# Kernel tuning notes

Hardware: AMD Instinct MI355X
Metric: run time of the kernel (lower is better)

## Reference

```python
import jax, jax.numpy as jnp
import numpy as np

EMB = 1024
HEADS = 16
HEAD_DIM = EMB // HEADS
MASK_VAL = -10000.0


def setup_inputs() -> dict:
    key = jax.random.key(0)
    ks = jax.random.split(key, 5)
    B, S = 4, 2048
    x = jax.random.normal(ks[0], (B, S, EMB), dtype=jnp.float32)
    scale = 1.0 / np.sqrt(EMB)
    w_qkv = jax.random.normal(ks[1], (EMB, 3 * EMB), dtype=jnp.float32) * scale
    b_qkv = jnp.zeros((3 * EMB,), dtype=jnp.float32)
    w_fc = jax.random.normal(ks[2], (EMB, EMB), dtype=jnp.float32) * scale
    b_fc = jnp.zeros((EMB,), dtype=jnp.float32)
    return {"x": x, "w_qkv": w_qkv, "b_qkv": b_qkv, "w_fc": w_fc, "b_fc": b_fc}


def reference(x, w_qkv, b_qkv, w_fc, b_fc):
    B, S, _ = x.shape
    qkv = x @ w_qkv + b_qkv                      # (B, S, 3*EMB)
    q, k, v = jnp.split(qkv, 3, axis=-1)
    # split heads: (B, S, EMB) -> (B, H, S, Dh)
    def sh(t):
        return t.reshape(B, S, HEADS, HEAD_DIM).transpose(0, 2, 1, 3)
    q, k, v = sh(q), sh(k), sh(v)
    scores = jnp.einsum('bhqd,bhkd->bhqk', q, k) / np.sqrt(HEAD_DIM)
    causal = jnp.tril(jnp.ones((S, S), dtype=bool))[None, None]
    scores = jnp.where(causal, scores, jnp.float32(MASK_VAL))
    probs = jax.nn.softmax(scores, axis=-1)
    out = jnp.einsum('bhqk,bhkd->bhqd', probs, v)
    out = out.transpose(0, 2, 1, 3).reshape(B, S, EMB)  # merge heads
    return out @ w_fc + b_fc
```

## Files before the change

kernel.cpp:

```cpp
#include <hip/hip_runtime.h>
#include <hip/hip_bf16.h>
#include <cstdint>

#define BF16 __hip_bfloat16

typedef __attribute__((ext_vector_type(8))) short bhalf8;
typedef __attribute__((ext_vector_type(4))) float floatx4;

#define MFMA16(a, b, c) __builtin_amdgcn_mfma_f32_16x16x32_bf16((a), (b), (c), 0, 0, 0)

#define MASKV (-30000.0f)
#define QSCALE 0.18033688011112042f

__device__ __forceinline__ bhalf8 cvt8(const float* p) {
  const float4 f0 = *(const float4*)p;
  const float4 f1 = *(const float4*)(p + 4);
  union { bhalf8 v; ushort u[8]; } r;
  const float t[8] = {f0.x, f0.y, f0.z, f0.w, f1.x, f1.y, f1.z, f1.w};
#pragma unroll
  for (int i = 0; i < 8; ++i) {
    BF16 h = __float2bfloat16(t[i]);
    r.u[i] = *(const ushort*)&h;
  }
  return r.v;
}

__global__ void cvt_f32_bf16(const float* __restrict__ in, BF16* __restrict__ out) {
  const size_t i = ((size_t)blockIdx.x * 256 + threadIdx.x) * 8;
  *(bhalf8*)(out + i) = cvt8(in + i);
}

__global__ void transpose_cvt(const float* __restrict__ in, ushort* __restrict__ out,
                              int R, int C) {
  __shared__ ushort t[32][33];
  const int c0 = blockIdx.x * 32, r0 = blockIdx.y * 32;
  const int tx = threadIdx.x, ty = threadIdx.y;
#pragma unroll
  for (int j = 0; j < 32; j += 8) {
    BF16 h = __float2bfloat16(in[(size_t)(r0 + ty + j) * C + c0 + tx]);
    t[ty + j][tx] = *(const ushort*)&h;
  }
  __syncthreads();
#pragma unroll
  for (int j = 0; j < 32; j += 8)
    out[(size_t)(c0 + ty + j) * R + r0 + tx] = t[tx][ty + j];
}

template <int MODE>
__global__ __launch_bounds__(256, 2) void gemm_bt(
    const BF16* __restrict__ A, const BF16* __restrict__ Bt, const float* __restrict__ bias,
    void* __restrict__ C0v, BF16* __restrict__ C1, BF16* __restrict__ C2,
    int Md, int Nd, int Kd) {
  __shared__ __align__(16) BF16 As[128 * 64];
  __shared__ __align__(16) BF16 Bs[128 * 64];

  const int tid = threadIdx.x;
  const int w = tid >> 6, lane = tid & 63;
  const int lm = lane & 15, quad = lane >> 4;
  const int wm = (w >> 1) * 64, wn = (w & 1) * 64;
  const int tile_m = blockIdx.y * 128, tile_n = blockIdx.x * 128;

  floatx4 acc[4][4];
#pragma unroll
  for (int i = 0; i < 4; ++i)
#pragma unroll
    for (int j = 0; j < 4; ++j) acc[i][j] = (floatx4){0.f, 0.f, 0.f, 0.f};

  int srow[4], sgs[4], sslot[4];
#pragma unroll
  for (int j = 0; j < 4; ++j) {
    const int slot = (j * 4 + w) * 64 + lane;
    sslot[j] = slot;
    srow[j] = slot >> 3;
    sgs[j] = ((slot & 7) - (slot >> 3)) & 7;
  }

  bhalf8 va[4], vb[4], nva[4], nvb[4];
#pragma unroll
  for (int j = 0; j < 4; ++j) {
    va[j] = *(const bhalf8*)(A + (size_t)(tile_m + srow[j]) * Kd + sgs[j] * 8);
    vb[j] = *(const bhalf8*)(Bt + (size_t)(tile_n + srow[j]) * Kd + sgs[j] * 8);
  }

  for (int k0 = 0; k0 < Kd; k0 += 64) {
    __syncthreads();
#pragma unroll
    for (int j = 0; j < 4; ++j) {
      *(bhalf8*)(As + sslot[j] * 8) = va[j];
      *(bhalf8*)(Bs + sslot[j] * 8) = vb[j];
    }
    __syncthreads();

    if (k0 + 64 < Kd) {
      const int k1 = k0 + 64;
#pragma unroll
      for (int j = 0; j < 4; ++j) {
        nva[j] = *(const bhalf8*)(A + (size_t)(tile_m + srow[j]) * Kd + k1 + sgs[j] * 8);
        nvb[j] = *(const bhalf8*)(Bt + (size_t)(tile_n + srow[j]) * Kd + k1 + sgs[j] * 8);
      }
    }

#pragma unroll
    for (int s = 0; s < 2; ++s) {
      bhalf8 af[4], bfr[4];
#pragma unroll
      for (int mt = 0; mt < 4; ++mt) {
        const int r = wm + mt * 16 + lm;
        const int g = ((s * 4 + quad) + r) & 7;
        af[mt] = *(const bhalf8*)(As + r * 64 + g * 8);
      }
#pragma unroll
      for (int nt = 0; nt < 4; ++nt) {
        const int r = wn + nt * 16 + lm;
        const int g = ((s * 4 + quad) + r) & 7;
        bfr[nt] = *(const bhalf8*)(Bs + r * 64 + g * 8);
      }
#pragma unroll
      for (int mt = 0; mt < 4; ++mt)
#pragma unroll
        for (int nt = 0; nt < 4; ++nt)
          acc[mt][nt] = MFMA16(af[mt], bfr[nt], acc[mt][nt]);
    }
#pragma unroll
    for (int j = 0; j < 4; ++j) { va[j] = nva[j]; vb[j] = nvb[j]; }
  }

#pragma unroll
  for (int nt = 0; nt < 4; ++nt) {
    const int n = tile_n + wn + nt * 16 + lm;
    const float bv = bias[n];
#pragma unroll
    for (int mt = 0; mt < 4; ++mt) {
      const int m0 = tile_m + wm + mt * 16 + quad * 4;
      floatx4 v = acc[mt][nt];
      if (MODE == 0) {
        float* C0f = (float*)C0v;
#pragma unroll
        for (int r = 0; r < 4; ++r)
          C0f[(size_t)(m0 + r) * Nd + n] = v[r] + bv;
      } else {
        const int which = n >> 10;
        const int h = (n >> 6) & 15;
        const int d = n & 63;
        if (which == 2) {
          const int b = m0 >> 11, s0 = m0 & 2047;
          union { ushort4 u4; ushort u[4]; } pk;
#pragma unroll
          for (int r = 0; r < 4; ++r) {
            BF16 hv = __float2bfloat16(v[r] + bv);
            pk.u[r] = *(const ushort*)&hv;
          }
          *(ushort4*)(C2 + ((size_t)((b * 16 + h) * 64 + d)) * 2048 + s0) = pk.u4;
        } else {
          BF16* dst = (which == 0) ? (BF16*)C0v : C1;
          const float sc = (which == 0) ? QSCALE : 1.0f;
#pragma unroll
          for (int r = 0; r < 4; ++r) {
            const int m = m0 + r, b = m >> 11, si = m & 2047;
            dst[((size_t)(b * 16 + h) * 2048 + si) * 64 + d] =
                __float2bfloat16((v[r] + bv) * sc);
          }
        }
      }
    }
  }
}

__global__ __launch_bounds__(256, 2) void flash_attn(
    const BF16* __restrict__ Q, const BF16* __restrict__ Kmat,
    const BF16* __restrict__ VT, BF16* __restrict__ O) {
  __shared__ __align__(16) BF16 Ks[64 * 64];
  __shared__ __align__(16) BF16 Vs[64 * 64];
  __shared__ __align__(16) BF16 Ps[4 * 16 * 64];

  const int bh = blockIdx.y;
  const int qt = (int)gridDim.x - 1 - (int)blockIdx.x;
  const int tid = threadIdx.x;
  const int w = tid >> 6, lane = tid & 63;
  const int lm = lane & 15, quad = lane >> 4;
  const size_t bh_off = (size_t)bh * (2048 * 64);

  const int qrow = qt * 64 + w * 16 + lm;
  const bhalf8 aq0 = *(const bhalf8*)(Q + bh_off + (size_t)qrow * 64 + quad * 8);
  const bhalf8 aq1 = *(const bhalf8*)(Q + bh_off + (size_t)qrow * 64 + 32 + quad * 8);

  floatx4 oacc[4];
#pragma unroll
  for (int i = 0; i < 4; ++i) oacc[i] = (floatx4){0.f, 0.f, 0.f, 0.f};
  float m_i = MASKV, l_i = 0.f;

  int srow[2], sgs[2], sslot[2];
#pragma unroll
  for (int j = 0; j < 2; ++j) {
    const int slot = (w * 2 + j) * 64 + lane;
    sslot[j] = slot;
    srow[j] = slot >> 3;
    sgs[j] = ((slot & 7) - (slot >> 3)) & 7;
  }
  BF16* pw = Ps + w * (16 * 64);

  bhalf8 kv[2], vv[2], nkv[2], nvv[2];
  {
    const BF16* Kg = Kmat + bh_off;
    const BF16* Vg = VT + bh_off;
#pragma unroll
    for (int j = 0; j < 2; ++j) {
      kv[j] = *(const bhalf8*)(Kg + srow[j] * 64 + sgs[j] * 8);
      vv[j] = *(const bhalf8*)(Vg + (size_t)srow[j] * 2048 + sgs[j] * 8);
    }
  }

  for (int kt = 0; kt <= qt; ++kt) {
    __syncthreads();
#pragma unroll
    for (int j = 0; j < 2; ++j) {
      *(bhalf8*)(Ks + sslot[j] * 8) = kv[j];
      *(bhalf8*)(Vs + sslot[j] * 8) = vv[j];
    }
    __syncthreads();

    if (kt < qt) {
      const BF16* Kg = Kmat + bh_off + (size_t)((kt + 1) * 64) * 64;
      const BF16* Vg = VT + bh_off + (kt + 1) * 64;
#pragma unroll
      for (int j = 0; j < 2; ++j) {
        nkv[j] = *(const bhalf8*)(Kg + srow[j] * 64 + sgs[j] * 8);
        nvv[j] = *(const bhalf8*)(Vg + (size_t)srow[j] * 2048 + sgs[j] * 8);
      }
    }

    floatx4 st[4];
#pragma unroll
    for (int nt = 0; nt < 4; ++nt) {
      const int rr = nt * 16 + lm;
      const bhalf8 ak0 = *(const bhalf8*)(Ks + rr * 64 + ((quad + rr) & 7) * 8);
      const bhalf8 ak1 = *(const bhalf8*)(Ks + rr * 64 + ((4 + quad + rr) & 7) * 8);
      floatx4 z = (floatx4){0.f, 0.f, 0.f, 0.f};
      z = MFMA16(ak0, aq0, z);
      z = MFMA16(ak1, aq1, z);
      st[nt] = z;
    }

    if (kt == qt) {
#pragma unroll
      for (int nt = 0; nt < 4; ++nt)
#pragma unroll
        for (int r = 0; r < 4; ++r)
          if ((nt * 16 + quad * 4 + r) > (w * 16 + lm)) st[nt][r] = MASKV;
    }

    float mx = MASKV;
#pragma unroll
    for (int nt = 0; nt < 4; ++nt)
#pragma unroll
      for (int r = 0; r < 4; ++r) mx = fmaxf(mx, st[nt][r]);
    mx = fmaxf(mx, __shfl_xor(mx, 16, 64));
    mx = fmaxf(mx, __shfl_xor(mx, 32, 64));
    const float mnew = fmaxf(m_i, mx);
    const float alpha = __builtin_amdgcn_exp2f(m_i - mnew);
    m_i = mnew;

    float rs = 0.f;
#pragma unroll
    for (int nt = 0; nt < 4; ++nt)
#pragma unroll
      for (int r = 0; r < 4; ++r) {
        const float p = __builtin_amdgcn_exp2f(st[nt][r] - mnew);
        st[nt][r] = p;
        rs += p;
      }
    rs += __shfl_xor(rs, 16, 64);
    rs += __shfl_xor(rs, 32, 64);
    l_i = l_i * alpha + rs;
#pragma unroll
    for (int dn = 0; dn < 4; ++dn) oacc[dn] *= alpha;

#pragma unroll
    for (int nt = 0; nt < 4; ++nt) {
      union { ushort4 u4; ushort u[4]; } pk;
#pragma unroll
      for (int r = 0; r < 4; ++r) {
        BF16 h = __float2bfloat16(st[nt][r]);
        pk.u[r] = *(const ushort*)&h;
      }
      const int g = ((nt * 2 + (quad >> 1)) + lm) & 7;
      *(ushort4*)(pw + lm * 64 + g * 8 + (quad & 1) * 4) = pk.u4;
    }

    const bhalf8 ap0 = *(const bhalf8*)(pw + lm * 64 + ((quad + lm) & 7) * 8);
    const bhalf8 ap1 = *(const bhalf8*)(pw + lm * 64 + ((4 + quad + lm) & 7) * 8);
#pragma unroll
    for (int dn = 0; dn < 4; ++dn) {
      const int rr = dn * 16 + lm;
      const bhalf8 av0 = *(const bhalf8*)(Vs + rr * 64 + ((quad + rr) & 7) * 8);
      const bhalf8 av1 = *(const bhalf8*)(Vs + rr * 64 + ((4 + quad + rr) & 7) * 8);
      oacc[dn] = MFMA16(av0, ap0, oacc[dn]);
      oacc[dn] = MFMA16(av1, ap1, oacc[dn]);
    }

#pragma unroll
    for (int j = 0; j < 2; ++j) { kv[j] = nkv[j]; vv[j] = nvv[j]; }
  }

  const int b = bh >> 4, h = bh & 15;
  const float inv_l = 1.0f / l_i;
#pragma unroll
  for (int dn = 0; dn < 4; ++dn) {
    union { ushort4 u4; ushort u[4]; } pk;
#pragma unroll
    for (int r = 0; r < 4; ++r) {
      BF16 h2 = __float2bfloat16(oacc[dn][r] * inv_l);
      pk.u[r] = *(const ushort*)&h2;
    }
    *(ushort4*)(O + ((size_t)(b * 2048 + qt * 64 + w * 16 + lm)) * 1024 +
                h * 64 + dn * 16 + quad * 4) = pk.u4;
  }
}

extern "C" void kernel_launch(void* const* d_in, const int* in_sizes, int n_in,
                              void* d_out, int out_size, void* d_ws, size_t ws_size,
                              hipStream_t stream) {
  const float* x = (const float*)d_in[0];
  const float* w_qkv = (const float*)d_in[1];
  const float* b_qkv = (const float*)d_in[2];
  const float* w_fc = (const float*)d_in[3];
  const float* b_fc = (const float*)d_in[4];
  float* out = (float*)d_out;

  BF16* ws = (BF16*)d_ws;
  BF16* wTqkv = ws;
  BF16* wTfc = wTqkv + 3072 * 1024;
  BF16* xb = wTfc + 1024 * 1024;
  BF16* Qb = xb + 8388608;
  BF16* Kb = Qb + 8388608;
  BF16* VTb = Kb + 8388608;
  BF16* Ob = VTb + 8388608;

  cvt_f32_bf16<<<4096, 256, 0, stream>>>(x, xb);
  transpose_cvt<<<dim3(96, 32), dim3(32, 8), 0, stream>>>(w_qkv, (ushort*)wTqkv, 1024, 3072);
  transpose_cvt<<<dim3(32, 32), dim3(32, 8), 0, stream>>>(w_fc, (ushort*)wTfc, 1024, 1024);

  gemm_bt<1><<<dim3(24, 64), 256, 0, stream>>>(
      xb, wTqkv, b_qkv, (void*)Qb, Kb, VTb, 8192, 3072, 1024);
  flash_attn<<<dim3(32, 64), 256, 0, stream>>>(Qb, Kb, VTb, Ob);
  gemm_bt<0><<<dim3(8, 64), 256, 0, stream>>>(
      Ob, wTfc, b_fc, (void*)out, nullptr, nullptr, 8192, 1024, 1024);
}
```

Before: 294.0 us.

## Use async global-to-LDS loads in GEMM and 128-row query tiles in attention

The GEMM now loads its A and B tiles straight into LDS with global_load_lds. This replaces the register-staged path that prefetched the next K-slice while the current one was computing. The flash-attention kernel now gives each block 128 query rows and each wave 32 rows in two 16-row sub-tiles. That halves K/V tile loads per query row and doubles MFMA work per LDS tile, at the cost of more registers, a larger P buffer, and coarser causal load balance. The GEMM loses its explicit prefetch overlap and depends on the barrier waiting for the async LDS writes.

New measurement: 309.3 us. 5.2% more time.

```diff
diff --git a/kernel.cpp b/kernel.cpp
--- a/kernel.cpp
+++ b/kernel.cpp
@@ -11,6 +11,12 @@
 
 #define MASKV (-30000.0f)
 #define QSCALE 0.18033688011112042f
+
+__device__ __forceinline__ void async_cp16(const void* gsrc, void* ldst) {
+  __builtin_amdgcn_global_load_lds(
+      (__attribute__((address_space(1))) void*)(size_t)gsrc,
+      (__attribute__((address_space(3))) void*)ldst, 16, 0, 0);
+}
 
 __device__ __forceinline__ bhalf8 cvt8(const float* p) {
   const float4 f0 = *(const float4*)p;
@@ -66,39 +72,18 @@
 #pragma unroll
     for (int j = 0; j < 4; ++j) acc[i][j] = (floatx4){0.f, 0.f, 0.f, 0.f};
 
-  int srow[4], sgs[4], sslot[4];
-#pragma unroll
-  for (int j = 0; j < 4; ++j) {
-    const int slot = (j * 4 + w) * 64 + lane;
-    sslot[j] = slot;
-    srow[j] = slot >> 3;
-    sgs[j] = ((slot & 7) - (slot >> 3)) & 7;
-  }
-
-  bhalf8 va[4], vb[4], nva[4], nvb[4];
-#pragma unroll
-  for (int j = 0; j < 4; ++j) {
-    va[j] = *(const bhalf8*)(A + (size_t)(tile_m + srow[j]) * Kd + sgs[j] * 8);
-    vb[j] = *(const bhalf8*)(Bt + (size_t)(tile_n + srow[j]) * Kd + sgs[j] * 8);
-  }
-
   for (int k0 = 0; k0 < Kd; k0 += 64) {
     __syncthreads();
 #pragma unroll
     for (int j = 0; j < 4; ++j) {
-      *(bhalf8*)(As + sslot[j] * 8) = va[j];
-      *(bhalf8*)(Bs + sslot[j] * 8) = vb[j];
+      const int sb = (j * 4 + w) * 64;
+      const int slot = sb + lane;
+      const int row = slot >> 3;
+      const int gs = ((slot & 7) - row) & 7;
+      async_cp16(A + (size_t)(tile_m + row) * Kd + k0 + gs * 8, As + sb * 8);
+      async_cp16(Bt + (size_t)(tile_n + row) * Kd + k0 + gs * 8, Bs + sb * 8);
     }
     __syncthreads();
-
-    if (k0 + 64 < Kd) {
-      const int k1 = k0 + 64;
-#pragma unroll
-      for (int j = 0; j < 4; ++j) {
-        nva[j] = *(const bhalf8*)(A + (size_t)(tile_m + srow[j]) * Kd + k1 + sgs[j] * 8);
-        nvb[j] = *(const bhalf8*)(Bt + (size_t)(tile_n + srow[j]) * Kd + k1 + sgs[j] * 8);
-      }
-    }
 
 #pragma unroll
     for (int s = 0; s < 2; ++s) {
@@ -121,8 +106,6 @@
         for (int nt = 0; nt < 4; ++nt)
           acc[mt][nt] = MFMA16(af[mt], bfr[nt], acc[mt][nt]);
     }
-#pragma unroll
-    for (int j = 0; j < 4; ++j) { va[j] = nva[j]; vb[j] = nvb[j]; }
   }
 
 #pragma unroll
@@ -171,7 +154,7 @@
     const BF16* __restrict__ VT, BF16* __restrict__ O) {
   __shared__ __align__(16) BF16 Ks[64 * 64];
   __shared__ __align__(16) BF16 Vs[64 * 64];
-  __shared__ __align__(16) BF16 Ps[4 * 16 * 64];
+  __shared__ __align__(16) BF16 Ps[4 * 32 * 64];
 
   const int bh = blockIdx.y;
   const int qt = (int)gridDim.x - 1 - (int)blockIdx.x;
@@ -180,14 +163,25 @@
   const int lm = lane & 15, quad = lane >> 4;
   const size_t bh_off = (size_t)bh * (2048 * 64);
 
-  const int qrow = qt * 64 + w * 16 + lm;
-  const bhalf8 aq0 = *(const bhalf8*)(Q + bh_off + (size_t)qrow * 64 + quad * 8);
-  const bhalf8 aq1 = *(const bhalf8*)(Q + bh_off + (size_t)qrow * 64 + 32 + quad * 8);
-
-  floatx4 oacc[4];
-#pragma unroll
-  for (int i = 0; i < 4; ++i) oacc[i] = (floatx4){0.f, 0.f, 0.f, 0.f};
-  float m_i = MASKV, l_i = 0.f;
+  const int qb0 = qt * 128 + w * 32;
+
+  bhalf8 aq[2][2];
+#pragma unroll
+  for (int s2 = 0; s2 < 2; ++s2) {
+    const size_t qoff = bh_off + (size_t)(qb0 + s2 * 16 + lm) * 64;
+    aq[s2][0] = *(const bhalf8*)(Q + qoff + quad * 8);
+    aq[s2][1] = *(const bhalf8*)(Q + qoff + 32 + quad * 8);
+  }
+
+  floatx4 oacc[2][4];
+  float m_i[2], l_i[2];
+#pragma unroll
+  for (int s2 = 0; s2 < 2; ++s2) {
+    m_i[s2] = MASKV;
+    l_i[s2] = 0.f;
+#pragma unroll
+    for (int i = 0; i < 4; ++i) oacc[s2][i] = (floatx4){0.f, 0.f, 0.f, 0.f};
+  }
 
   int srow[2], sgs[2], sslot[2];
 #pragma unroll
@@ -197,7 +191,7 @@
     srow[j] = slot >> 3;
     sgs[j] = ((slot & 7) - (slot >> 3)) & 7;
   }
-  BF16* pw = Ps + w * (16 * 64);
+  BF16* pw = Ps + w * (32 * 64);
 
   bhalf8 kv[2], vv[2], nkv[2], nvv[2];
   {
@@ -210,7 +204,8 @@
     }
   }
 
-  for (int kt = 0; kt <= qt; ++kt) {
+  const int ktmax = 2 * qt + 1;
+  for (int kt = 0; kt <= ktmax; ++kt) {
     __syncthreads();
 #pragma unroll
     for (int j = 0; j < 2; ++j) {
@@ -219,7 +214,7 @@
     }
     __syncthreads();
 
-    if (kt < qt) {
+    if (kt < ktmax) {
       const BF16* Kg = Kmat + bh_off + (size_t)((kt + 1) * 64) * 64;
       const BF16* Vg = VT + bh_off + (kt + 1) * 64;
 #pragma unroll
@@ -229,91 +224,102 @@
       }
     }
 
-    floatx4 st[4];
-#pragma unroll
-    for (int nt = 0; nt < 4; ++nt) {
-      const int rr = nt * 16 + lm;
-      const bhalf8 ak0 = *(const bhalf8*)(Ks + rr * 64 + ((quad + rr) & 7) * 8);
-      const bhalf8 ak1 = *(const bhalf8*)(Ks + rr * 64 + ((4 + quad + rr) & 7) * 8);
-      floatx4 z = (floatx4){0.f, 0.f, 0.f, 0.f};
-      z = MFMA16(ak0, aq0, z);
-      z = MFMA16(ak1, aq1, z);
-      st[nt] = z;
-    }
-
-    if (kt == qt) {
+    const int k0 = kt * 64;
+#pragma unroll
+    for (int s2 = 0; s2 < 2; ++s2) {
+      const int qb = qb0 + s2 * 16;
+      if (k0 > qb + 15) continue;
+
+      floatx4 st[4];
+#pragma unroll
+      for (int nt = 0; nt < 4; ++nt) {
+        const int rr = nt * 16 + lm;
+        const bhalf8 ak0 = *(const bhalf8*)(Ks + rr * 64 + ((quad + rr) & 7) * 8);
+        const bhalf8 ak1 = *(const bhalf8*)(Ks + rr * 64 + ((4 + quad + rr) & 7) * 8);
+        floatx4 z = (floatx4){0.f, 0.f, 0.f, 0.f};
+        z = MFMA16(ak0, aq[s2][0], z);
+        z = MFMA16(ak1, aq[s2][1], z);
+        st[nt] = z;
+      }
+
+      if (k0 + 63 > qb) {
+#pragma unroll
+        for (int nt = 0; nt < 4; ++nt)
+#pragma unroll
+          for (int r = 0; r < 4; ++r)
+            if ((k0 + nt * 16 + quad * 4 + r) > (qb + lm)) st[nt][r] = MASKV;
+      }
+
+      float mx = MASKV;
 #pragma unroll
       for (int nt = 0; nt < 4; ++nt)
 #pragma unroll
-        for (int r = 0; r < 4; ++r)
-          if ((nt * 16 + quad * 4 + r) > (w * 16 + lm)) st[nt][r] = MASKV;
-    }
-
-    float mx = MASKV;
-#pragma unroll
-    for (int nt = 0; nt < 4; ++nt)
-#pragma unroll
-      for (int r = 0; r < 4; ++r) mx = fmaxf(mx, st[nt][r]);
-    mx = fmaxf(mx, __shfl_xor(mx, 16, 64));
-    mx = fmaxf(mx, __shfl_xor(mx, 32, 64));
-    const float mnew = fmaxf(m_i, mx);
-    const float alpha = __builtin_amdgcn_exp2f(m_i - mnew);
-    m_i = mnew;
-
-    float rs = 0.f;
-#pragma unroll
-    for (int nt = 0; nt < 4; ++nt)
+        for (int r = 0; r < 4; ++r) mx = fmaxf(mx, st[nt][r]);
+      mx = fmaxf(mx, __shfl_xor(mx, 16, 64));
+      mx = fmaxf(mx, __shfl_xor(mx, 32, 64));
+      const float mnew = fmaxf(m_i[s2], mx);
+      const float alpha = __builtin_amdgcn_exp2f(m_i[s2] - mnew);
+      m_i[s2] = mnew;
+
+      float rs = 0.f;
+#pragma unroll
+      for (int nt = 0; nt < 4; ++nt)
+#pragma unroll
+        for (int r = 0; r < 4; ++r) {
+          const float p = __builtin_amdgcn_exp2f(st[nt][r] - mnew);
+          st[nt][r] = p;
+          rs += p;
+        }
+      rs += __shfl_xor(rs, 16, 64);
+      rs += __shfl_xor(rs, 32, 64);
+      l_i[s2] = l_i[s2] * alpha + rs;
+#pragma unroll
+      for (int dn = 0; dn < 4; ++dn) oacc[s2][dn] *= alpha;
+
+      BF16* pws = pw + s2 * (16 * 64);
+#pragma unroll
+      for (int nt = 0; nt < 4; ++nt) {
+        union { ushort4 u4; ushort u[4]; } pk;
+#pragma unroll
+        for (int r = 0; r < 4; ++r) {
+          BF16 h = __float2bfloat16(st[nt][r]);
+          pk.u[r] = *(const ushort*)&h;
+        }
+        const int g = ((nt * 2 + (quad >> 1)) + lm) & 7;
+        *(ushort4*)(pws + lm * 64 + g * 8 + (quad & 1) * 4) = pk.u4;
+      }
+
+      const bhalf8 ap0 = *(const bhalf8*)(pws + lm * 64 + ((quad + lm) & 7) * 8);
+      const bhalf8 ap1 = *(const bhalf8*)(pws + lm * 64 + ((4 + quad + lm) & 7) * 8);
+#pragma unroll
+      for (int dn = 0; dn < 4; ++dn) {
+        const int rr = dn * 16 + lm;
+        const bhalf8 av0 = *(const bhalf8*)(Vs + rr * 64 + ((quad + rr) & 7) * 8);
+        const bhalf8 av1 = *(const bhalf8*)(Vs + rr * 64 + ((4 + quad + rr) & 7) * 8);
+        oacc[s2][dn] = MFMA16(av0, ap0, oacc[s2][dn]);
+        oacc[s2][dn] = MFMA16(av1, ap1, oacc[s2][dn]);
+      }
+    }
+
+#pragma unroll
+    for (int j = 0; j < 2; ++j) { kv[j] = nkv[j]; vv[j] = nvv[j]; }
+  }
+
+  const int b = bh >> 4, h = bh & 15;
+#pragma unroll
+  for (int s2 = 0; s2 < 2; ++s2) {
+    const float inv_l = 1.0f / l_i[s2];
+    const size_t orow = (size_t)(b * 2048 + qb0 + s2 * 16 + lm) * 1024 + h * 64;
+#pragma unroll
+    for (int dn = 0; dn < 4; ++dn) {
+      union { ushort4 u4; ushort u[4]; } pk;
 #pragma unroll
       for (int r = 0; r < 4; ++r) {
-        const float p = __builtin_amdgcn_exp2f(st[nt][r] - mnew);
-        st[nt][r] = p;
-        rs += p;
-      }
-    rs += __shfl_xor(rs, 16, 64);
-    rs += __shfl_xor(rs, 32, 64);
-    l_i = l_i * alpha + rs;
-#pragma unroll
-    for (int dn = 0; dn < 4; ++dn) oacc[dn] *= alpha;
-
-#pragma unroll
-    for (int nt = 0; nt < 4; ++nt) {
-      union { ushort4 u4; ushort u[4]; } pk;
-#pragma unroll
-      for (int r = 0; r < 4; ++r) {
-        BF16 h = __float2bfloat16(st[nt][r]);
-        pk.u[r] = *(const ushort*)&h;
-      }
-      const int g = ((nt * 2 + (quad >> 1)) + lm) & 7;
-      *(ushort4*)(pw + lm * 64 + g * 8 + (quad & 1) * 4) = pk.u4;
-    }
-
-    const bhalf8 ap0 = *(const bhalf8*)(pw + lm * 64 + ((quad + lm) & 7) * 8);
-    const bhalf8 ap1 = *(const bhalf8*)(pw + lm * 64 + ((4 + quad + lm) & 7) * 8);
-#pragma unroll
-    for (int dn = 0; dn < 4; ++dn) {
-      const int rr = dn * 16 + lm;
-      const bhalf8 av0 = *(const bhalf8*)(Vs + rr * 64 + ((quad + rr) & 7) * 8);
-      const bhalf8 av1 = *(const bhalf8*)(Vs + rr * 64 + ((4 + quad + rr) & 7) * 8);
-      oacc[dn] = MFMA16(av0, ap0, oacc[dn]);
-      oacc[dn] = MFMA16(av1, ap1, oacc[dn]);
-    }
-
-#pragma unroll
-    for (int j = 0; j < 2; ++j) { kv[j] = nkv[j]; vv[j] = nvv[j]; }
-  }
-
-  const int b = bh >> 4, h = bh & 15;
-  const float inv_l = 1.0f / l_i;
-#pragma unroll
-  for (int dn = 0; dn < 4; ++dn) {
-    union { ushort4 u4; ushort u[4]; } pk;
-#pragma unroll
-    for (int r = 0; r < 4; ++r) {
-      BF16 h2 = __float2bfloat16(oacc[dn][r] * inv_l);
-      pk.u[r] = *(const ushort*)&h2;
-    }
-    *(ushort4*)(O + ((size_t)(b * 2048 + qt * 64 + w * 16 + lm)) * 1024 +
-                h * 64 + dn * 16 + quad * 4) = pk.u4;
+        BF16 h2 = __float2bfloat16(oacc[s2][dn][r] * inv_l);
+        pk.u[r] = *(const ushort*)&h2;
+      }
+      *(ushort4*)(O + orow + dn * 16 + quad * 4) = pk.u4;
+    }
   }
 }
 
@@ -342,7 +348,7 @@
 
   gemm_bt<1><<<dim3(24, 64), 256, 0, stream>>>(
       xb, wTqkv, b_qkv, (void*)Qb, Kb, VTb, 8192, 3072, 1024);
-  flash_attn<<<dim3(32, 64), 256, 0, stream>>>(Qb, Kb, VTb, Ob);
+  flash_attn<<<dim3(16, 64), 256, 0, stream>>>(Qb, Kb, VTb, Ob);
   gemm_bt<0><<<dim3(8, 64), 256, 0, stream>>>(
       Ob, wTfc, b_fc, (void*)out, nullptr, nullptr, 8192, 1024, 1024);
 }
```
